# Kernel optimization log

Hardware: AMD Instinct MI355X
Metric: run time of the kernel (lower is better)

## Reference

```python
import jax, jax.numpy as jnp
import numpy as np

NEG = -1e9  # max-semiring 'zero' / structural mask value


def _cky_max(pot, lengths):
    """Max-plus CKY inside pass (torch_struct CKY_CRF with MaxSemiring).

    pot: [B, N, N] label-maxed span potentials, pot[b, i, j] = score of span (i, j).
    Returns [B] best binary-tree score for each sequence of given length.
    betaA[b, i, w]      = best score of span starting at i with width w (span [i, i+w]).
    betaB[b, j, N-1-w]  = best score of span ending at j with width w.
    """
    B, N, _ = pot.shape
    term = jnp.diagonal(pot, axis1=1, axis2=2)  # [B, N] width-0 spans
    betaA = jnp.full((B, N, N), NEG, dtype=pot.dtype).at[:, :, 0].set(term)
    betaB = jnp.full((B, N, N), NEG, dtype=pot.dtype).at[:, :, N - 1].set(term)
    for w in range(1, N):
        Y = betaA[:, : N - w, :w]       # [B, N-w, w] left children, widths 0..w-1
        Z = betaB[:, w:, N - w:]        # [B, N-w, w] right children (matching splits)
        span = jnp.diagonal(pot, offset=w, axis1=1, axis2=2)  # [B, N-w] pot[b, i, i+w]
        new = jnp.max(Y + Z, axis=-1) + span
        betaA = betaA.at[:, : N - w, w].set(new)
        betaB = betaB.at[:, w:, N - w - 1].set(new)
    final = betaA[:, 0, :]  # [B, N]: final[b, l-1] = best tree over [0, l-1]
    return final[jnp.arange(B), lengths - 1]


def setup_inputs() -> dict:
    key = jax.random.key(0)
    k1, k2 = jax.random.split(key)
    B, N, L = 64, 128, 32
    logits = jax.random.normal(k1, (B, N, N, L), dtype=jnp.float32)
    labels = jax.random.randint(k2, (B, N, N), 0, L, dtype=jnp.int64)
    return {"logits": logits, "labels": labels}


def reference(logits, labels):
    B, N, _, L = logits.shape
    gold_event = jax.nn.one_hot(jnp.maximum(labels, 0), L, dtype=logits.dtype)
    logits = logits - logits[..., :1]
    lengths = jnp.sum(labels[:, 0, :] != -100, axis=-1)
    augment = 1.0 - gold_event
    # force_root_constituent=True: forbid non-constituent root span
    augment = augment.at[jnp.arange(B), 0, lengths - 1, 0].add(-1e9)
    pot = jnp.max(logits + augment, axis=-1)  # max-semiring sum over label dim
    pred_score = _cky_max(pot, lengths)                      # [B]
    gold_score = jnp.sum(logits * gold_event, axis=(1, 2, 3))  # [B]
    margin_losses = jax.nn.relu(pred_score - gold_score)
    return jnp.mean(margin_losses)
```

## Files before the change

kernel.cpp:

```cpp
#include <hip/hip_runtime.h>

#define BATCH 64
#define SEQ   128
#define NLAB  32
#define NEGF  -3.0e38f

__global__ __launch_bounds__(64) void len_kernel(
    const int* __restrict__ labels, int* __restrict__ lenbuf)
{
    const int b = blockIdx.x;
    const int t = threadIdx.x;
    const size_t base = (size_t)b * SEQ * SEQ;
    int cnt = (labels[base + t] != -100) + (labels[base + 64 + t] != -100);
    #pragma unroll
    for (int d = 32; d; d >>= 1) cnt += __shfl_down(cnt, d, 64);
    if (t == 0) lenbuf[b] = cnt;
}

__global__ __launch_bounds__(256) void pot_gold_kernel(
    const float* __restrict__ logits, const int* __restrict__ labels,
    const int* __restrict__ lenbuf,
    float* __restrict__ pot, float* __restrict__ gold)
{
    const int tid = threadIdx.x;
    const int wave = tid >> 6, lane = tid & 63;
    __shared__ __align__(16) float LP[4 * 16 * 36];
    float* W = LP + wave * (16 * 36);

    const int block_cell0 = blockIdx.x * 256;
    const int b = block_cell0 >> 14;
    const int len = lenbuf[b];
    float gacc = 0.0f;

    const int wave_cell0 = block_cell0 + wave * 64;

    #pragma unroll
    for (int chunk = 0; chunk < 4; ++chunk) {
        const int c0 = wave_cell0 + chunk * 16;
        const float4* src = reinterpret_cast<const float4*>(logits) + ((size_t)c0 << 3);
        const float4 f0 = src[lane];
        const float4 f1 = src[lane + 64];
        const int lv = (lane < 16) ? labels[c0 + lane] : 0;

        {
            const int cA = lane >> 3, tA = lane & 7;
            *reinterpret_cast<float4*>(W + cA * 36 + tA * 4) = f0;
            const int q1 = lane + 64;
            const int cB = q1 >> 3, tB = q1 & 7;
            *reinterpret_cast<float4*>(W + cB * 36 + tB * 4) = f1;
        }
        const int c = lane >> 2, u = lane & 3;
        const float4 r0 = *reinterpret_cast<const float4*>(W + c * 36 + u * 8);
        const float4 r1 = *reinterpret_cast<const float4*>(W + c * 36 + u * 8 + 4);

        int lab = __shfl(lv, c, 64);
        if (lab < 0) lab = 0;
        const float l0 = __shfl(r0.x, c << 2, 64);

        const int cell = c0 + c;
        const int ci = (cell >> 7) & (SEQ - 1);
        const int cj = cell & (SEQ - 1);
        const bool special = (ci == 0) && (cj == len - 1);

        const float vv[8] = { r0.x, r0.y, r0.z, r0.w, r1.x, r1.y, r1.z, r1.w };
        float m = NEGF, g = 0.0f;
        #pragma unroll
        for (int e = 0; e < 8; ++e) {
            const int l = u * 8 + e;
            const float r = vv[e] - l0;
            const bool isg = (l == lab);
            g = isg ? r : g;
            float cand = r + (isg ? 0.0f : 1.0f);
            if (l == 0 && special) cand -= 1.0e9f;
            m = fmaxf(m, cand);
        }
        m = fmaxf(m, __shfl_xor(m, 1, 64));
        m = fmaxf(m, __shfl_xor(m, 2, 64));
        g += __shfl_xor(g, 1, 64);
        g += __shfl_xor(g, 2, 64);
        if (u == 0) {
            pot[cell] = m;
            gacc += g;
        }
    }

    #pragma unroll
    for (int d = 1; d < 64; d <<= 1) gacc += __shfl_xor(gacc, d, 64);
    __shared__ float gred[4];
    if (lane == 0) gred[wave] = gacc;
    __syncthreads();
    if (tid == 0)
        atomicAdd(&gold[b], gred[0] + gred[1] + gred[2] + gred[3]);
}

template<int TPE, int LT>
__device__ __forceinline__ void cky_step(
    float* __restrict__ A, float* __restrict__ Bt, const int w, const int tid)
{
    const int entries = SEQ - w;
    const int i = tid >> LT;
    const int s = tid & (TPE - 1);
    if (i < entries) {
        float* Arow = A + i * 132;
        const int j = i + w;
        const float potv = Arow[w];
        const int wq = (w + 3) >> 2;
        float m = NEGF;
        #pragma unroll 4
        for (int q = s; q < wq; q += TPE) {
            const int k0 = q << 2;
            float4 a = *reinterpret_cast<const float4*>(Arow + k0);
            const int r0 = w - 1 - k0;
            const float b0 = Bt[r0 * 130 + j];
            const float b1 = Bt[(r0 > 1 ? r0 - 1 : 0) * 130 + j];
            const float b2 = Bt[(r0 > 2 ? r0 - 2 : 0) * 130 + j];
            const float b3 = Bt[(r0 > 3 ? r0 - 3 : 0) * 130 + j];
            a.y = (k0 + 1 < w) ? a.y : NEGF;
            a.z = (k0 + 2 < w) ? a.z : NEGF;
            a.w = (k0 + 3 < w) ? a.w : NEGF;
            m = fmaxf(m, fmaxf(fmaxf(a.x + b0, a.y + b1),
                               fmaxf(a.z + b2, a.w + b3)));
        }
        #pragma unroll
        for (int d = TPE >> 1; d; d >>= 1)
            m = fmaxf(m, __shfl_down(m, d, TPE));
        if (s == 0) {
            const float val = m + potv;
            Arow[w] = val;
            Bt[w * 130 + j] = val;
        }
    }
    __syncthreads();
}

__global__ __launch_bounds__(512, 1) void cky_kernel(
    const float* __restrict__ pot, const float* __restrict__ gold,
    const int* __restrict__ lenbuf, float* __restrict__ out)
{
    const int b = blockIdx.x;
    const int tid = threadIdx.x;
    const float* p = pot + (size_t)b * SEQ * SEQ;

    __shared__ __align__(16) float A[SEQ * 132];
    __shared__ __align__(16) float Bt[SEQ * 130];

    {
        const float4 neg4 = make_float4(NEGF, NEGF, NEGF, NEGF);
        float4* a4 = reinterpret_cast<float4*>(A);
        for (int idx = tid; idx < SEQ * 132 / 4; idx += 512) a4[idx] = neg4;
    }
    __syncthreads();
    {
        const float4* p4 = reinterpret_cast<const float4*>(p);
        for (int qi = tid; qi < SEQ * SEQ / 4; qi += 512) {
            const int i = qi >> 5;
            const int j0 = (qi & 31) << 2;
            const float4 v = p4[qi];
            const float vv[4] = { v.x, v.y, v.z, v.w };
            #pragma unroll
            for (int c2 = 0; c2 < 4; ++c2) {
                const int j = j0 + c2;
                if (j >= i) {
                    A[i * 132 + (j - i)] = vv[c2];
                    Bt[(j - i) * 130 + j] = vv[c2];
                }
            }
        }
    }
    __syncthreads();

    for (int w = 1;  w < 16;  ++w) cky_step<1, 0>(A, Bt, w, tid);
    for (int w = 16; w < 32;  ++w) cky_step<2, 1>(A, Bt, w, tid);
    for (int w = 32; w < 64;  ++w) cky_step<4, 2>(A, Bt, w, tid);
    for (int w = 64; w < SEQ; ++w) cky_step<8, 3>(A, Bt, w, tid);

    if (tid == 0) {
        const int len = lenbuf[b];
        const float pred = A[len - 1];
        float margin = pred - gold[b];
        margin = margin > 0.0f ? margin : 0.0f;
        atomicAdd(out, margin * (1.0f / (float)BATCH));
    }
}

extern "C" void kernel_launch(void* const* d_in, const int* in_sizes, int n_in,
                              void* d_out, int out_size, void* d_ws, size_t ws_size,
                              hipStream_t stream) {
    const float* logits = (const float*)d_in[0];
    const int* labels = (const int*)d_in[1];
    float* out = (float*)d_out;

    float* pot = (float*)d_ws;
    float* gold = pot + (size_t)BATCH * SEQ * SEQ;
    int* lenbuf = (int*)(gold + BATCH);

    (void)hipMemsetAsync(out, 0, sizeof(float), stream);
    (void)hipMemsetAsync(gold, 0, BATCH * sizeof(float), stream);

    len_kernel<<<BATCH, 64, 0, stream>>>(labels, lenbuf);
    pot_gold_kernel<<<BATCH * SEQ * SEQ / 256, 256, 0, stream>>>(
        logits, labels, lenbuf, pot, gold);
    cky_kernel<<<BATCH, 512, 0, stream>>>(pot, gold, lenbuf, out);
}
```

Baseline: 267.9 us.

## Store CKY right-child table row-major per end index for vectorized LDS reads

Result: faster. 261.7 us (-2.3%).

```diff
diff --git a/kernel.cpp b/kernel.cpp
--- a/kernel.cpp
+++ b/kernel.cpp
@@ -6,7 +6,8 @@
 #define NEGF  -3.0e38f
 
 __global__ __launch_bounds__(64) void len_kernel(
-    const int* __restrict__ labels, int* __restrict__ lenbuf)
+    const int* __restrict__ labels, int* __restrict__ lenbuf,
+    float* __restrict__ gold)
 {
     const int b = blockIdx.x;
     const int t = threadIdx.x;
@@ -14,7 +15,7 @@
     int cnt = (labels[base + t] != -100) + (labels[base + 64 + t] != -100);
     #pragma unroll
     for (int d = 32; d; d >>= 1) cnt += __shfl_down(cnt, d, 64);
-    if (t == 0) lenbuf[b] = cnt;
+    if (t == 0) { lenbuf[b] = cnt; gold[b] = 0.0f; }
 }
 
 __global__ __launch_bounds__(256) void pot_gold_kernel(
@@ -93,7 +94,7 @@
         atomicAdd(&gold[b], gred[0] + gred[1] + gred[2] + gred[3]);
 }
 
-template<int TPE, int LT>
+template<int TPE, int LT, int S>
 __device__ __forceinline__ void cky_step(
     float* __restrict__ A, float* __restrict__ Bt, const int w, const int tid)
 {
@@ -103,6 +104,7 @@
     if (i < entries) {
         float* Arow = A + i * 132;
         const int j = i + w;
+        const float* Brow = Bt + j * 132 + (SEQ - w);
         const float potv = Arow[w];
         const int wq = (w + 3) >> 2;
         float m = NEGF;
@@ -110,11 +112,21 @@
         for (int q = s; q < wq; q += TPE) {
             const int k0 = q << 2;
             float4 a = *reinterpret_cast<const float4*>(Arow + k0);
-            const int r0 = w - 1 - k0;
-            const float b0 = Bt[r0 * 130 + j];
-            const float b1 = Bt[(r0 > 1 ? r0 - 1 : 0) * 130 + j];
-            const float b2 = Bt[(r0 > 2 ? r0 - 2 : 0) * 130 + j];
-            const float b3 = Bt[(r0 > 3 ? r0 - 3 : 0) * 130 + j];
+            const float* bp = Brow + k0;
+            float b0, b1, b2, b3;
+            if (S == 0) {
+                const float4 bv = *reinterpret_cast<const float4*>(bp);
+                b0 = bv.x; b1 = bv.y; b2 = bv.z; b3 = bv.w;
+            } else if (S == 2) {
+                const float2 u0 = *reinterpret_cast<const float2*>(bp);
+                const float2 u1 = *reinterpret_cast<const float2*>(bp + 2);
+                b0 = u0.x; b1 = u0.y; b2 = u1.x; b3 = u1.y;
+            } else {
+                b0 = bp[0];
+                const float2 u = *reinterpret_cast<const float2*>(bp + 1);
+                b1 = u.x; b2 = u.y;
+                b3 = bp[3];
+            }
             a.y = (k0 + 1 < w) ? a.y : NEGF;
             a.z = (k0 + 2 < w) ? a.z : NEGF;
             a.w = (k0 + 3 < w) ? a.w : NEGF;
@@ -127,10 +139,20 @@
         if (s == 0) {
             const float val = m + potv;
             Arow[w] = val;
-            Bt[w * 130 + j] = val;
-        }
-    }
-    __syncthreads();
+            Bt[j * 132 + (SEQ - 1 - w)] = val;
+        }
+    }
+    __syncthreads();
+}
+
+template<int TPE, int LT>
+__device__ __forceinline__ void cky_phase4(
+    float* __restrict__ A, float* __restrict__ Bt, const int w, const int tid)
+{
+    cky_step<TPE, LT, 0>(A, Bt, w,     tid);
+    cky_step<TPE, LT, 3>(A, Bt, w + 1, tid);
+    cky_step<TPE, LT, 2>(A, Bt, w + 2, tid);
+    cky_step<TPE, LT, 1>(A, Bt, w + 3, tid);
 }
 
 __global__ __launch_bounds__(512, 1) void cky_kernel(
@@ -142,12 +164,15 @@
     const float* p = pot + (size_t)b * SEQ * SEQ;
 
     __shared__ __align__(16) float A[SEQ * 132];
-    __shared__ __align__(16) float Bt[SEQ * 130];
+    __shared__ __align__(16) float Bt[SEQ * 132];
 
     {
         const float4 neg4 = make_float4(NEGF, NEGF, NEGF, NEGF);
         float4* a4 = reinterpret_cast<float4*>(A);
-        for (int idx = tid; idx < SEQ * 132 / 4; idx += 512) a4[idx] = neg4;
+        float4* b4 = reinterpret_cast<float4*>(Bt);
+        for (int idx = tid; idx < SEQ * 132 / 4; idx += 512) {
+            a4[idx] = neg4; b4[idx] = neg4;
+        }
     }
     __syncthreads();
     {
@@ -162,17 +187,20 @@
                 const int j = j0 + c2;
                 if (j >= i) {
                     A[i * 132 + (j - i)] = vv[c2];
-                    Bt[(j - i) * 130 + j] = vv[c2];
+                    Bt[j * 132 + (SEQ - 1 - (j - i))] = vv[c2];
                 }
             }
         }
     }
     __syncthreads();
 
-    for (int w = 1;  w < 16;  ++w) cky_step<1, 0>(A, Bt, w, tid);
-    for (int w = 16; w < 32;  ++w) cky_step<2, 1>(A, Bt, w, tid);
-    for (int w = 32; w < 64;  ++w) cky_step<4, 2>(A, Bt, w, tid);
-    for (int w = 64; w < SEQ; ++w) cky_step<8, 3>(A, Bt, w, tid);
+    cky_step<1, 0, 3>(A, Bt, 1, tid);
+    cky_step<1, 0, 2>(A, Bt, 2, tid);
+    cky_step<1, 0, 1>(A, Bt, 3, tid);
+    for (int w = 4;  w < 16;  w += 4) cky_phase4<1, 0>(A, Bt, w, tid);
+    for (int w = 16; w < 32;  w += 4) cky_phase4<2, 1>(A, Bt, w, tid);
+    for (int w = 32; w < 64;  w += 4) cky_phase4<4, 2>(A, Bt, w, tid);
+    for (int w = 64; w < SEQ; w += 4) cky_phase4<8, 3>(A, Bt, w, tid);
 
     if (tid == 0) {
         const int len = lenbuf[b];
@@ -195,9 +223,8 @@
     int* lenbuf = (int*)(gold + BATCH);
 
     (void)hipMemsetAsync(out, 0, sizeof(float), stream);
-    (void)hipMemsetAsync(gold, 0, BATCH * sizeof(float), stream);
-
-    len_kernel<<<BATCH, 64, 0, stream>>>(labels, lenbuf);
+
+    len_kernel<<<BATCH, 64, 0, stream>>>(labels, lenbuf, gold);
     pot_gold_kernel<<<BATCH * SEQ * SEQ / 256, 256, 0, stream>>>(
         logits, labels, lenbuf, pot, gold);
     cky_kernel<<<BATCH, 512, 0, stream>>>(pot, gold, lenbuf, out);
```
